# Kernel tuning notes

Measured on AMD Instinct MI355X. Metric: run time of the kernel, lower is better.

The kernel has to match this reference:

```python
import jax, jax.numpy as jnp
import numpy as np

N = 1_048_576
C = 64
K = 20
BN_EPS = 1e-3
IGNORE = -1


def setup_inputs() -> dict:
    key = jax.random.key(0)
    ks = jax.random.split(key, 8)
    feat = jax.random.normal(ks[0], (N, C), dtype=jnp.float32)
    coord = jax.random.uniform(ks[1], (N, 3), dtype=jnp.float32) * 10.0
    segment = jax.random.randint(ks[2], (N,), 0, K).astype(jnp.int32)
    instance = jax.random.randint(ks[3], (N,), 0, 500).astype(jnp.int32)
    instance_centroid = jax.random.uniform(ks[4], (N, 3), dtype=jnp.float32) * 10.0
    W1 = jax.random.normal(ks[5], (C, C), dtype=jnp.float32) * 0.05
    b1 = jnp.zeros((C,), jnp.float32)
    gamma = jnp.ones((C,), jnp.float32)
    beta = jnp.zeros((C,), jnp.float32)
    W2 = jax.random.normal(ks[6], (C, 3), dtype=jnp.float32) * 0.05
    b2 = jnp.zeros((3,), jnp.float32)
    Wseg = jax.random.normal(ks[7], (C, K), dtype=jnp.float32) * 0.05
    bseg = jnp.zeros((K,), jnp.float32)
    class_weights = jnp.ones((K,), jnp.float32)
    return dict(feat=feat, coord=coord, segment=segment, instance=instance,
                instance_centroid=instance_centroid, W1=W1, b1=b1, gamma=gamma,
                beta=beta, W2=W2, b2=b2, Wseg=Wseg, bseg=bseg,
                class_weights=class_weights)


def _heads(feat, W1, b1, gamma, beta, W2, b2, Wseg, bseg):
    # bias_head: Linear -> BatchNorm1d(train-mode batch stats, eps=1e-3) -> ReLU -> Linear
    h = feat @ W1 + b1                      # [N, C]
    mean = jnp.mean(h, axis=0)
    var = jnp.var(h, axis=0)                # biased var, matching torch BN
    h = (h - mean) * jax.lax.rsqrt(var + BN_EPS) * gamma + beta
    h = jax.nn.relu(h)
    bias_pred = h @ W2 + b2                 # [N, 3]
    logit_pred = feat @ Wseg + bseg         # [N, K]
    return logit_pred, bias_pred


def reference(feat, coord, segment, instance, instance_centroid,
              W1, b1, gamma, beta, W2, b2, Wseg, bseg, class_weights):
    logit_pred, bias_pred = _heads(feat, W1, b1, gamma, beta, W2, b2, Wseg, bseg)

    # weighted CrossEntropyLoss with ignore_index, torch semantics:
    # sum(w_t * nll) / sum(w_t) over non-ignored targets
    valid = (segment != IGNORE)
    tgt = jnp.where(valid, segment, 0)
    logp = jax.nn.log_softmax(logit_pred, axis=-1)
    nll = -jnp.take_along_axis(logp, tgt[:, None], axis=1)[:, 0]
    w = class_weights[tgt] * valid.astype(logp.dtype)
    seg_loss = jnp.sum(w * nll) / jnp.sum(w)

    mask = (instance != IGNORE).astype(bias_pred.dtype)
    denom = jnp.sum(mask) + 1e-8
    bias_gt = instance_centroid - coord
    bias_dist = jnp.sum(jnp.abs(bias_pred - bias_gt), axis=-1)
    bias_l1_loss = jnp.sum(bias_dist * mask) / denom

    pred_norm = bias_pred / (jnp.linalg.norm(bias_pred, axis=1, keepdims=True) + 1e-8)
    gt_norm = bias_gt / (jnp.linalg.norm(bias_gt, axis=1, keepdims=True) + 1e-8)
    cos = -jnp.sum(pred_norm * gt_norm, axis=-1)
    bias_cosine_loss = jnp.sum(cos * mask) / denom

    loss = seg_loss + bias_l1_loss + bias_cosine_loss
    return jnp.stack([loss, seg_loss, bias_l1_loss, bias_cosine_loss])
```

## Files before the change

### kernel.cpp

```cpp
#include <hip/hip_runtime.h>
#include <math.h>

#define C 64
#define K 20
#define TPB 256
#define ROWS_PER_TILE 128
#define NT 8
#define ASTR 72

#define NB 8
#define BSTR 512
#define SCOFF (NB * BSTR)
#define HOFF 18432

#define P1_TPB 128
#define P1_ROWS 128
#define LSTR 65

typedef __attribute__((ext_vector_type(8))) short bf16x8;
typedef __attribute__((ext_vector_type(4))) float f32x4;


__device__ __forceinline__ float wave_reduce_add(float v) {
#pragma unroll
  for (int m = 32; m > 0; m >>= 1) v += __shfl_xor(v, m, 64);
  return v;
}

__device__ __forceinline__ unsigned short f2bf16(float x) {
  union { float f; unsigned u; } v; v.f = x;
  unsigned r = v.u + 0x7FFFu + ((v.u >> 16) & 1u);
  return (unsigned short)(r >> 16);
}

__device__ __forceinline__ bf16x8 cvt8(float4 lo, float4 hi) {
  bf16x8 r;
  r[0] = (short)f2bf16(lo.x); r[1] = (short)f2bf16(lo.y);
  r[2] = (short)f2bf16(lo.z); r[3] = (short)f2bf16(lo.w);
  r[4] = (short)f2bf16(hi.x); r[5] = (short)f2bf16(hi.y);
  r[6] = (short)f2bf16(hi.z); r[7] = (short)f2bf16(hi.w);
  return r;
}



__global__ __launch_bounds__(TPB, 4)
void pass1_kernel(const float* __restrict__ feat,
                  const int* __restrict__ segment,
                  const float* __restrict__ W1,
                  const float* __restrict__ Wseg,
                  const float* __restrict__ bseg,
                  const float* __restrict__ cw,
                  float* __restrict__ ws,
                  unsigned short* __restrict__ hout,
                  int store_h, int n) {
  __shared__ __align__(16) unsigned short Bs[96 * ASTR];
  __shared__ float cred[512];
  __shared__ float wpart[8];

  const int t = threadIdx.x;
  const int wv = t >> 6;
  const int L = t & 63;
  const int colL = L & 15;
  const int quad = L >> 4;
  const long long blockbase = (long long)blockIdx.x * (ROWS_PER_TILE * NT);
  const int rbase = wv * 32;

  float* bucket = ws + (blockIdx.x & (NB - 1)) * BSTR;

  float s1[4] = {0, 0, 0, 0}, s2[4] = {0, 0, 0, 0};
  float wnll = 0.f, wsum = 0.f;

  const float bsega = bseg[colL];
  const float bsegb = (colL < 4) ? bseg[16 + colL] : 0.f;

  float4 af[8];
  auto issue_tile = [&](int it) {
    const long long trow = blockbase + (long long)it * ROWS_PER_TILE + rbase;
    const float* frow = feat + (trow + colL) * C + quad * 8;
#pragma unroll
    for (int rt = 0; rt < 2; ++rt)
#pragma unroll
      for (int kh = 0; kh < 2; ++kh) {
        const float* p = frow + rt * (16 * C) + kh * 32;
        af[rt * 4 + kh * 2 + 0] = *(const float4*)p;
        af[rt * 4 + kh * 2 + 1] = *(const float4*)(p + 4);
      }
  };

  issue_tile(0);

#pragma unroll
  for (int i = 0; i < 16; ++i) {
    int e = t + i * 256;
    Bs[(e & 63) * ASTR + (e >> 6)] = f2bf16(W1[e]);
  }
#pragma unroll
  for (int i = 0; i < 8; ++i) {
    int e = t + i * 256;
    int k = e >> 5, j = e & 31;
    float v = (j < K) ? Wseg[k * K + j] : 0.0f;
    Bs[(64 + j) * ASTR + k] = f2bf16(v);
  }
  __syncthreads();

  for (int it = 0; it < NT; ++it) {
    int segc[8];
    {
      const long long trow = blockbase + (long long)it * ROWS_PER_TILE + rbase;
#pragma unroll
      for (int rt = 0; rt < 2; ++rt)
#pragma unroll
        for (int r = 0; r < 4; ++r)
          segc[rt * 4 + r] = segment[trow + rt * 16 + quad * 4 + r];
    }

    bf16x8 a[2][2];
#pragma unroll
    for (int rt = 0; rt < 2; ++rt)
#pragma unroll
      for (int kh = 0; kh < 2; ++kh)
        a[rt][kh] = cvt8(af[rt * 4 + kh * 2], af[rt * 4 + kh * 2 + 1]);
    if (it + 1 < NT) issue_tile(it + 1);

    f32x4 ah[2][4];
#pragma unroll
    for (int rt = 0; rt < 2; ++rt)
#pragma unroll
      for (int ct = 0; ct < 4; ++ct) ah[rt][ct] = (f32x4){0.f, 0.f, 0.f, 0.f};
#pragma unroll
    for (int kh = 0; kh < 2; ++kh) {
      const int k0 = kh * 32 + quad * 8;
#pragma unroll
      for (int ct = 0; ct < 4; ++ct) {
        bf16x8 b = *(const bf16x8*)(Bs + (ct * 16 + colL) * ASTR + k0);
        ah[0][ct] = __builtin_amdgcn_mfma_f32_16x16x32_bf16(a[0][kh], b, ah[0][ct], 0, 0, 0);
        ah[1][ct] = __builtin_amdgcn_mfma_f32_16x16x32_bf16(a[1][kh], b, ah[1][ct], 0, 0, 0);
      }
    }

    {
      unsigned short* uso = hout + (long long)(blockIdx.x * NT + it) * 8192 + wv * 2048;
#pragma unroll
      for (int rt = 0; rt < 2; ++rt)
#pragma unroll
        for (int ct = 0; ct < 4; ++ct) {
          float v0 = ah[rt][ct][0], v1 = ah[rt][ct][1];
          float v2 = ah[rt][ct][2], v3 = ah[rt][ct][3];
          s1[ct] += v0 + v1 + v2 + v3;
          s2[ct] = __builtin_fmaf(v0, v0, s2[ct]);
          s2[ct] = __builtin_fmaf(v1, v1, s2[ct]);
          s2[ct] = __builtin_fmaf(v2, v2, s2[ct]);
          s2[ct] = __builtin_fmaf(v3, v3, s2[ct]);
          if (store_h) {
            ushort4 o;
            o.x = f2bf16(v0); o.y = f2bf16(v1); o.z = f2bf16(v2); o.w = f2bf16(v3);
            *(ushort4*)(uso + (rt * 4 + ct) * 256 + L * 4) = o;
          }
        }
    }

    f32x4 alg[2][2];
#pragma unroll
    for (int rt = 0; rt < 2; ++rt)
#pragma unroll
      for (int cc = 0; cc < 2; ++cc) alg[rt][cc] = (f32x4){0.f, 0.f, 0.f, 0.f};
#pragma unroll
    for (int kh = 0; kh < 2; ++kh) {
      const int k0 = kh * 32 + quad * 8;
#pragma unroll
      for (int cc = 0; cc < 2; ++cc) {
        bf16x8 b = *(const bf16x8*)(Bs + ((4 + cc) * 16 + colL) * ASTR + k0);
        alg[0][cc] = __builtin_amdgcn_mfma_f32_16x16x32_bf16(a[0][kh], b, alg[0][cc], 0, 0, 0);
        alg[1][cc] = __builtin_amdgcn_mfma_f32_16x16x32_bf16(a[1][kh], b, alg[1][cc], 0, 0, 0);
      }
    }

#pragma unroll
    for (int rt = 0; rt < 2; ++rt)
#pragma unroll
      for (int r = 0; r < 4; ++r) {
        float la = alg[rt][0][r] + bsega;
        float lb = (colL < 4) ? alg[rt][1][r] + bsegb : -3.0e38f;
        const int sg = segc[rt * 4 + r];
        const bool valid = (sg != -1);
        const int tgt = valid ? sg : 0;
        float mx = fmaxf(la, lb);
        mx = fmaxf(mx, __shfl_xor(mx, 1, 64));
        mx = fmaxf(mx, __shfl_xor(mx, 2, 64));
        mx = fmaxf(mx, __shfl_xor(mx, 4, 64));
        mx = fmaxf(mx, __shfl_xor(mx, 8, 64));
        float e = __expf(la - mx) + ((colL < 4) ? __expf(lb - mx) : 0.f);
        float tp = ((colL == tgt) ? la : 0.f) + ((colL + 16 == tgt) ? lb : 0.f);
#pragma unroll
        for (int m = 1; m <= 8; m <<= 1) {
          e += __shfl_xor(e, m, 64);
          tp += __shfl_xor(tp, m, 64);
        }
        float nll = mx + __logf(e) - tp;
        float wct = cw[tgt];
        if (colL == 0) {
          float w = valid ? wct : 0.f;
          wnll += w * nll;
          wsum += w;
        }
      }
  }

#pragma unroll
  for (int ct = 0; ct < 4; ++ct) {
    float a1 = s1[ct]; a1 += __shfl_xor(a1, 16, 64); a1 += __shfl_xor(a1, 32, 64);
    float a2 = s2[ct]; a2 += __shfl_xor(a2, 16, 64); a2 += __shfl_xor(a2, 32, 64);
    if (L < 16) { cred[wv * 64 + ct * 16 + colL] = a1; cred[256 + wv * 64 + ct * 16 + colL] = a2; }
  }
  {
    float rwn = wave_reduce_add(wnll);
    float rw = wave_reduce_add(wsum);
    if (L == 0) { wpart[wv * 2] = rwn; wpart[wv * 2 + 1] = rw; }
  }
  __syncthreads();
  if (t == 0) {
    atomicAdd(&bucket[0], wpart[0] + wpart[2] + wpart[4] + wpart[6]);
    atomicAdd(&bucket[1], wpart[1] + wpart[3] + wpart[5] + wpart[7]);
  }
  if (t < C) {
    float u1 = cred[t] + cred[64 + t] + cred[128 + t] + cred[192 + t];
    float u2 = cred[256 + t] + cred[320 + t] + cred[384 + t] + cred[448 + t];
    atomicAdd(&bucket[8 + t], u1);
    atomicAdd(&bucket[72 + t], u2);
  }
}


__global__ void prep_kernel(const float* __restrict__ gamma,
                            const float* __restrict__ beta,
                            float* __restrict__ ws, int n) {
  int j = threadIdx.x;
  float s1 = 0.f, s2 = 0.f;
#pragma unroll
  for (int b = 0; b < NB; ++b) { s1 += ws[b * BSTR + 8 + j]; s2 += ws[b * BSTR + 72 + j]; }
  float inv_n = 1.0f / (float)n;
  float mean = s1 * inv_n;
  float var = fmaxf(s2 * inv_n - mean * mean, 0.0f);
  float sc = gamma[j] * rsqrtf(var + 1e-3f);
  ws[SCOFF + j] = sc;
  ws[SCOFF + 64 + j] = beta[j] - mean * sc;
}


__global__ __launch_bounds__(TPB, 4)
void pass2_frag(const unsigned short* __restrict__ hsrc,
                const float* __restrict__ coord,
                const int* __restrict__ instance,
                const float* __restrict__ centroid,
                const float* __restrict__ W2,
                const float* __restrict__ b2,
                float* __restrict__ ws, int n) {
  __shared__ float part[4][3];
  const int t = threadIdx.x;
  const int w = t >> 6, L = t & 63;
  const int colL = L & 15, quad = L >> 4;
  float* bucket = ws + (blockIdx.x & (NB - 1)) * BSTR;

  const float* ssc = ws + SCOFF;
  const float* ssh = ws + SCOFF + 64;
  float scv[4], shv[4], w20[4], w21[4], w22[4];
#pragma unroll
  for (int ct = 0; ct < 4; ++ct) {
    int j = ct * 16 + colL;
    scv[ct] = ssc[j];
    shv[ct] = ssh[j];
    w20[ct] = W2[j * 3 + 0];
    w21[ct] = W2[j * 3 + 1];
    w22[ct] = W2[j * 3 + 2];
  }
  const float bb0 = b2[0], bb1 = b2[1], bb2 = b2[2];

  float l1a = 0.f, cosa = 0.f, ma = 0.f;

  ushort4 hv[8];
  auto issue_h = [&](int it) {
    const ushort4* src = (const ushort4*)(hsrc + (long long)(blockIdx.x * NT + it) * 8192 + w * 2048);
#pragma unroll
    for (int s = 0; s < 8; ++s) hv[s] = src[s * 64 + L];
  };
  float pc[2][3], pg[2][3]; int pin[2];
  auto issue_pts = [&](int it) {
    if (colL < 4) {
      const long long rowb = (long long)blockIdx.x * (ROWS_PER_TILE * NT) +
                             (long long)it * ROWS_PER_TILE + w * 32 + quad * 4 + colL;
#pragma unroll
      for (int rt = 0; rt < 2; ++rt) {
        long long p = rowb + rt * 16;
        pc[rt][0] = coord[p * 3 + 0]; pc[rt][1] = coord[p * 3 + 1]; pc[rt][2] = coord[p * 3 + 2];
        pg[rt][0] = centroid[p * 3 + 0]; pg[rt][1] = centroid[p * 3 + 1]; pg[rt][2] = centroid[p * 3 + 2];
        pin[rt] = instance[p];
      }
    }
  };

  issue_h(0);
  issue_pts(0);

  for (int it = 0; it < NT; ++it) {
    ushort4 hc[8];
#pragma unroll
    for (int s = 0; s < 8; ++s) hc[s] = hv[s];
    if (it + 1 < NT) issue_h(it + 1);

#pragma unroll
    for (int rt = 0; rt < 2; ++rt) {
      float d[12];
#pragma unroll
      for (int e = 0; e < 12; ++e) d[e] = 0.f;
#pragma unroll
      for (int ct = 0; ct < 4; ++ct) {
        ushort4 q = hc[rt * 4 + ct];
        unsigned short qa[4] = { q.x, q.y, q.z, q.w };
#pragma unroll
        for (int r = 0; r < 4; ++r) {
          float v = __uint_as_float((unsigned)qa[r] << 16);
          float y = fmaxf(__builtin_fmaf(v, scv[ct], shv[ct]), 0.0f);
          d[r * 3 + 0] = __builtin_fmaf(y, w20[ct], d[r * 3 + 0]);
          d[r * 3 + 1] = __builtin_fmaf(y, w21[ct], d[r * 3 + 1]);
          d[r * 3 + 2] = __builtin_fmaf(y, w22[ct], d[r * 3 + 2]);
        }
      }
#pragma unroll
      for (int m = 1; m <= 8; m <<= 1)
#pragma unroll
        for (int e = 0; e < 12; ++e) d[e] += __shfl_xor(d[e], m, 64);
      if (colL < 4) {
        const int r = colL;
        float bp0 = d[r * 3 + 0] + bb0;
        float bp1 = d[r * 3 + 1] + bb1;
        float bp2 = d[r * 3 + 2] + bb2;
        float gx = pg[rt][0] - pc[rt][0];
        float gy = pg[rt][1] - pc[rt][1];
        float gz = pg[rt][2] - pc[rt][2];
        float m = (pin[rt] != -1) ? 1.0f : 0.0f;
        float l1 = fabsf(bp0 - gx) + fabsf(bp1 - gy) + fabsf(bp2 - gz);
        float npn = sqrtf(bp0 * bp0 + bp1 * bp1 + bp2 * bp2) + 1e-8f;
        float ngn = sqrtf(gx * gx + gy * gy + gz * gz) + 1e-8f;
        float cs = -(bp0 * gx + bp1 * gy + bp2 * gz) / (npn * ngn);
        l1a += l1 * m;
        cosa += cs * m;
        ma += m;
      }
    }
    if (it + 1 < NT) issue_pts(it + 1);
  }

  float r0 = wave_reduce_add(l1a);
  float r1 = wave_reduce_add(cosa);
  float r2 = wave_reduce_add(ma);
  if (L == 0) { part[w][0] = r0; part[w][1] = r1; part[w][2] = r2; }
  __syncthreads();
  if (t == 0) {
    float a0 = 0, a1 = 0, a2 = 0;
#pragma unroll
    for (int k = 0; k < 4; ++k) { a0 += part[k][0]; a1 += part[k][1]; a2 += part[k][2]; }
    atomicAdd(&bucket[2], a0);
    atomicAdd(&bucket[3], a1);
    atomicAdd(&bucket[4], a2);
  }
}


__global__ __launch_bounds__(P1_TPB, 2)
void pass2_recompute(const float* __restrict__ feat,
                     const float* __restrict__ coord,
                     const int* __restrict__ instance,
                     const float* __restrict__ centroid,
                     const float* __restrict__ W1,
                     const float* __restrict__ W2,
                     const float* __restrict__ b2,
                     float* __restrict__ ws, int n) {
  __shared__ float lds[P1_ROWS * LSTR];
  __shared__ float part[2][3];
  const int tid = threadIdx.x;
  const int wave = tid >> 6;
  const int lane = tid & 63;
  const long long base = (long long)blockIdx.x * P1_ROWS;
  float* bucket = ws + (blockIdx.x & (NB - 1)) * BSTR;

  {
    const float4* src = (const float4*)(feat + base * C);
#pragma unroll
    for (int i = 0; i < 16; ++i) {
      int g = tid + i * P1_TPB;
      float4 v = src[g];
      float* d = &lds[(g >> 4) * LSTR + ((g & 15) << 2)];
      d[0] = v.x; d[1] = v.y; d[2] = v.z; d[3] = v.w;
    }
  }
  __syncthreads();

  float h[C];
#pragma unroll
  for (int j = 0; j < C; ++j) h[j] = 0.0f;
  const float* frow = &lds[tid * LSTR];
#pragma unroll 4
  for (int k = 0; k < C; ++k) {
    float fk = frow[k];
#pragma unroll
    for (int j = 0; j < C; ++j) h[j] = __builtin_fmaf(fk, W1[k * C + j], h[j]);
  }

  const float* ssc = ws + SCOFF;
  const float* ssh = ws + SCOFF + 64;
  float bp0 = b2[0], bp1 = b2[1], bp2 = b2[2];
#pragma unroll
  for (int j = 0; j < C; ++j) {
    float y = fmaxf(__builtin_fmaf(h[j], ssc[j], ssh[j]), 0.0f);
    bp0 = __builtin_fmaf(y, W2[j * 3 + 0], bp0);
    bp1 = __builtin_fmaf(y, W2[j * 3 + 1], bp1);
    bp2 = __builtin_fmaf(y, W2[j * 3 + 2], bp2);
  }

  const long long p = base + tid;
  float cx = coord[p * 3 + 0], cy = coord[p * 3 + 1], cz = coord[p * 3 + 2];
  float gx = centroid[p * 3 + 0] - cx;
  float gy = centroid[p * 3 + 1] - cy;
  float gz = centroid[p * 3 + 2] - cz;
  float m = (instance[p] != -1) ? 1.0f : 0.0f;
  float l1 = fabsf(bp0 - gx) + fabsf(bp1 - gy) + fabsf(bp2 - gz);
  float npn = sqrtf(bp0 * bp0 + bp1 * bp1 + bp2 * bp2) + 1e-8f;
  float ngn = sqrtf(gx * gx + gy * gy + gz * gz) + 1e-8f;
  float cs = -(bp0 * gx + bp1 * gy + bp2 * gz) / (npn * ngn);
  float r0 = wave_reduce_add(l1 * m);
  float r1 = wave_reduce_add(cs * m);
  float r2 = wave_reduce_add(m);
  if (lane == 0) { part[wave][0] = r0; part[wave][1] = r1; part[wave][2] = r2; }
  __syncthreads();
  if (tid == 0) {
    atomicAdd(&bucket[2], part[0][0] + part[1][0]);
    atomicAdd(&bucket[3], part[0][1] + part[1][1]);
    atomicAdd(&bucket[4], part[0][2] + part[1][2]);
  }
}


__global__ void finalize_kernel(const float* __restrict__ ws, float* __restrict__ out) {
  if (threadIdx.x == 0 && blockIdx.x == 0) {
    float a0 = 0, a1 = 0, a2 = 0, a3 = 0, a4 = 0;
#pragma unroll
    for (int b = 0; b < NB; ++b) {
      const float* bk = ws + b * BSTR;
      a0 += bk[0]; a1 += bk[1]; a2 += bk[2]; a3 += bk[3]; a4 += bk[4];
    }
    float seg = a0 / a1;
    float den = a4 + 1e-8f;
    float l1 = a2 / den;
    float cs = a3 / den;
    out[0] = seg + l1 + cs;
    out[1] = seg;
    out[2] = l1;
    out[3] = cs;
  }
}


extern "C" void kernel_launch(void* const* d_in, const int* in_sizes, int n_in,
                              void* d_out, int out_size, void* d_ws, size_t ws_size,
                              hipStream_t stream) {
  const float* feat = (const float*)d_in[0];
  const float* coord = (const float*)d_in[1];
  const int* segment = (const int*)d_in[2];
  const int* instance = (const int*)d_in[3];
  const float* centroid = (const float*)d_in[4];
  const float* W1 = (const float*)d_in[5];
  const float* gamma = (const float*)d_in[7];
  const float* beta = (const float*)d_in[8];
  const float* W2 = (const float*)d_in[9];
  const float* b2 = (const float*)d_in[10];
  const float* Wseg = (const float*)d_in[11];
  const float* bseg = (const float*)d_in[12];
  const float* cw = (const float*)d_in[13];

  const int n = in_sizes[0] / C;

  float* ws = (float*)d_ws;
  unsigned short* hbuf = (unsigned short*)((char*)d_ws + HOFF);
  const size_t need = (size_t)HOFF + (size_t)n * C * sizeof(unsigned short);
  const int store_h = (ws_size >= need) ? 1 : 0;

  size_t zbytes = ws_size < (size_t)(NB * BSTR * 4) ? ws_size : (size_t)(NB * BSTR * 4);
  hipMemsetAsync(d_ws, 0, zbytes, stream);

  const int nblk = n / (ROWS_PER_TILE * NT);
  pass1_kernel<<<nblk, TPB, 0, stream>>>(feat, segment, W1, Wseg, bseg, cw,
                                         ws, hbuf, store_h, n);
  prep_kernel<<<1, 64, 0, stream>>>(gamma, beta, ws, n);
  if (store_h) {
    pass2_frag<<<nblk, TPB, 0, stream>>>(hbuf, coord, instance, centroid,
                                         W2, b2, ws, n);
  } else {
    pass2_recompute<<<n / P1_ROWS, P1_TPB, 0, stream>>>(feat, coord, instance, centroid,
                                                        W1, W2, b2, ws, n);
  }
  finalize_kernel<<<1, 1, 0, stream>>>(ws, (float*)d_out);
}
```

Before: 564.1 us.

## Recompute BN-head hidden layer with MFMA in pass2 instead of storing bf16 h

Removes the bf16 h spill buffer that pass1 wrote and pass2 read back, and also removes the scalar-FMA recompute fallback. Pass2 now reloads feat, converts it to bf16 and recomputes feat@W1 with the same MFMA tiling pass1 uses before applying BN, ReLU and W2. This drops the write and read of an N×64 intermediate and the workspace-size dependence. In exchange it re-reads the full fp32 feat tensor and repeats the GEMM in pass2.

New measurement: 664.4 us. +17.8%, slower.

```diff
diff --git a/kernel.cpp b/kernel.cpp
--- a/kernel.cpp
+++ b/kernel.cpp
@@ -11,11 +11,6 @@
 #define NB 8
 #define BSTR 512
 #define SCOFF (NB * BSTR)
-#define HOFF 18432
-
-#define P1_TPB 128
-#define P1_ROWS 128
-#define LSTR 65
 
 typedef __attribute__((ext_vector_type(8))) short bf16x8;
 typedef __attribute__((ext_vector_type(4))) float f32x4;
@@ -51,9 +46,7 @@
                   const float* __restrict__ Wseg,
                   const float* __restrict__ bseg,
                   const float* __restrict__ cw,
-                  float* __restrict__ ws,
-                  unsigned short* __restrict__ hout,
-                  int store_h, int n) {
+                  float* __restrict__ ws, int n) {
   __shared__ __align__(16) unsigned short Bs[96 * ASTR];
   __shared__ float cred[512];
   __shared__ float wpart[8];
@@ -139,26 +132,18 @@
       }
     }
 
-    {
-      unsigned short* uso = hout + (long long)(blockIdx.x * NT + it) * 8192 + wv * 2048;
-#pragma unroll
-      for (int rt = 0; rt < 2; ++rt)
-#pragma unroll
-        for (int ct = 0; ct < 4; ++ct) {
-          float v0 = ah[rt][ct][0], v1 = ah[rt][ct][1];
-          float v2 = ah[rt][ct][2], v3 = ah[rt][ct][3];
-          s1[ct] += v0 + v1 + v2 + v3;
-          s2[ct] = __builtin_fmaf(v0, v0, s2[ct]);
-          s2[ct] = __builtin_fmaf(v1, v1, s2[ct]);
-          s2[ct] = __builtin_fmaf(v2, v2, s2[ct]);
-          s2[ct] = __builtin_fmaf(v3, v3, s2[ct]);
-          if (store_h) {
-            ushort4 o;
-            o.x = f2bf16(v0); o.y = f2bf16(v1); o.z = f2bf16(v2); o.w = f2bf16(v3);
-            *(ushort4*)(uso + (rt * 4 + ct) * 256 + L * 4) = o;
-          }
-        }
-    }
+#pragma unroll
+    for (int rt = 0; rt < 2; ++rt)
+#pragma unroll
+      for (int ct = 0; ct < 4; ++ct) {
+        float v0 = ah[rt][ct][0], v1 = ah[rt][ct][1];
+        float v2 = ah[rt][ct][2], v3 = ah[rt][ct][3];
+        s1[ct] += v0 + v1 + v2 + v3;
+        s2[ct] = __builtin_fmaf(v0, v0, s2[ct]);
+        s2[ct] = __builtin_fmaf(v1, v1, s2[ct]);
+        s2[ct] = __builtin_fmaf(v2, v2, s2[ct]);
+        s2[ct] = __builtin_fmaf(v3, v3, s2[ct]);
+      }
 
     f32x4 alg[2][2];
 #pragma unroll
@@ -249,17 +234,22 @@
 
 
 __global__ __launch_bounds__(TPB, 4)
-void pass2_frag(const unsigned short* __restrict__ hsrc,
+void pass2_mfma(const float* __restrict__ feat,
                 const float* __restrict__ coord,
                 const int* __restrict__ instance,
                 const float* __restrict__ centroid,
+                const float* __restrict__ W1,
                 const float* __restrict__ W2,
                 const float* __restrict__ b2,
                 float* __restrict__ ws, int n) {
+  __shared__ __align__(16) unsigned short Bs[64 * ASTR];
   __shared__ float part[4][3];
+
   const int t = threadIdx.x;
-  const int w = t >> 6, L = t & 63;
+  const int wv = t >> 6, L = t & 63;
   const int colL = L & 15, quad = L >> 4;
+  const long long blockbase = (long long)blockIdx.x * (ROWS_PER_TILE * NT);
+  const int rbase = wv * 32;
   float* bucket = ws + (blockIdx.x & (NB - 1)) * BSTR;
 
   const float* ssc = ws + SCOFF;
@@ -276,19 +266,24 @@
   }
   const float bb0 = b2[0], bb1 = b2[1], bb2 = b2[2];
 
-  float l1a = 0.f, cosa = 0.f, ma = 0.f;
-
-  ushort4 hv[8];
-  auto issue_h = [&](int it) {
-    const ushort4* src = (const ushort4*)(hsrc + (long long)(blockIdx.x * NT + it) * 8192 + w * 2048);
-#pragma unroll
-    for (int s = 0; s < 8; ++s) hv[s] = src[s * 64 + L];
+  float4 af[8];
+  auto issue_tile = [&](int it) {
+    const long long trow = blockbase + (long long)it * ROWS_PER_TILE + rbase;
+    const float* frow = feat + (trow + colL) * C + quad * 8;
+#pragma unroll
+    for (int rt = 0; rt < 2; ++rt)
+#pragma unroll
+      for (int kh = 0; kh < 2; ++kh) {
+        const float* p = frow + rt * (16 * C) + kh * 32;
+        af[rt * 4 + kh * 2 + 0] = *(const float4*)p;
+        af[rt * 4 + kh * 2 + 1] = *(const float4*)(p + 4);
+      }
   };
   float pc[2][3], pg[2][3]; int pin[2];
   auto issue_pts = [&](int it) {
     if (colL < 4) {
-      const long long rowb = (long long)blockIdx.x * (ROWS_PER_TILE * NT) +
-                             (long long)it * ROWS_PER_TILE + w * 32 + quad * 4 + colL;
+      const long long rowb = blockbase + (long long)it * ROWS_PER_TILE +
+                             rbase + quad * 4 + colL;
 #pragma unroll
       for (int rt = 0; rt < 2; ++rt) {
         long long p = rowb + rt * 16;
@@ -299,14 +294,43 @@
     }
   };
 
-  issue_h(0);
+  issue_tile(0);
+
+#pragma unroll
+  for (int i = 0; i < 16; ++i) {
+    int e = t + i * 256;
+    Bs[(e & 63) * ASTR + (e >> 6)] = f2bf16(W1[e]);
+  }
+  __syncthreads();
+
   issue_pts(0);
 
+  float l1a = 0.f, cosa = 0.f, ma = 0.f;
+
   for (int it = 0; it < NT; ++it) {
-    ushort4 hc[8];
-#pragma unroll
-    for (int s = 0; s < 8; ++s) hc[s] = hv[s];
-    if (it + 1 < NT) issue_h(it + 1);
+    bf16x8 a[2][2];
+#pragma unroll
+    for (int rt = 0; rt < 2; ++rt)
+#pragma unroll
+      for (int kh = 0; kh < 2; ++kh)
+        a[rt][kh] = cvt8(af[rt * 4 + kh * 2], af[rt * 4 + kh * 2 + 1]);
+    if (it + 1 < NT) issue_tile(it + 1);
+
+    f32x4 ah[2][4];
+#pragma unroll
+    for (int rt = 0; rt < 2; ++rt)
+#pragma unroll
+      for (int ct = 0; ct < 4; ++ct) ah[rt][ct] = (f32x4){0.f, 0.f, 0.f, 0.f};
+#pragma unroll
+    for (int kh = 0; kh < 2; ++kh) {
+      const int k0 = kh * 32 + quad * 8;
+#pragma unroll
+      for (int ct = 0; ct < 4; ++ct) {
+        bf16x8 b = *(const bf16x8*)(Bs + (ct * 16 + colL) * ASTR + k0);
+        ah[0][ct] = __builtin_amdgcn_mfma_f32_16x16x32_bf16(a[0][kh], b, ah[0][ct], 0, 0, 0);
+        ah[1][ct] = __builtin_amdgcn_mfma_f32_16x16x32_bf16(a[1][kh], b, ah[1][ct], 0, 0, 0);
+      }
+    }
 
 #pragma unroll
     for (int rt = 0; rt < 2; ++rt) {
@@ -315,11 +339,9 @@
       for (int e = 0; e < 12; ++e) d[e] = 0.f;
 #pragma unroll
       for (int ct = 0; ct < 4; ++ct) {
-        ushort4 q = hc[rt * 4 + ct];
-        unsigned short qa[4] = { q.x, q.y, q.z, q.w };
 #pragma unroll
         for (int r = 0; r < 4; ++r) {
-          float v = __uint_as_float((unsigned)qa[r] << 16);
+          float v = ah[rt][ct][r];
           float y = fmaxf(__builtin_fmaf(v, scv[ct], shv[ct]), 0.0f);
           d[r * 3 + 0] = __builtin_fmaf(y, w20[ct], d[r * 3 + 0]);
           d[r * 3 + 1] = __builtin_fmaf(y, w21[ct], d[r * 3 + 1]);
@@ -354,7 +376,7 @@
   float r0 = wave_reduce_add(l1a);
   float r1 = wave_reduce_add(cosa);
   float r2 = wave_reduce_add(ma);
-  if (L == 0) { part[w][0] = r0; part[w][1] = r1; part[w][2] = r2; }
+  if (L == 0) { part[wv][0] = r0; part[wv][1] = r1; part[wv][2] = r2; }
   __syncthreads();
   if (t == 0) {
     float a0 = 0, a1 = 0, a2 = 0;
@@ -363,80 +385,6 @@
     atomicAdd(&bucket[2], a0);
     atomicAdd(&bucket[3], a1);
     atomicAdd(&bucket[4], a2);
-  }
-}
-
-
-__global__ __launch_bounds__(P1_TPB, 2)
-void pass2_recompute(const float* __restrict__ feat,
-                     const float* __restrict__ coord,
-                     const int* __restrict__ instance,
-                     const float* __restrict__ centroid,
-                     const float* __restrict__ W1,
-                     const float* __restrict__ W2,
-                     const float* __restrict__ b2,
-                     float* __restrict__ ws, int n) {
-  __shared__ float lds[P1_ROWS * LSTR];
-  __shared__ float part[2][3];
-  const int tid = threadIdx.x;
-  const int wave = tid >> 6;
-  const int lane = tid & 63;
-  const long long base = (long long)blockIdx.x * P1_ROWS;
-  float* bucket = ws + (blockIdx.x & (NB - 1)) * BSTR;
-
-  {
-    const float4* src = (const float4*)(feat + base * C);
-#pragma unroll
-    for (int i = 0; i < 16; ++i) {
-      int g = tid + i * P1_TPB;
-      float4 v = src[g];
-      float* d = &lds[(g >> 4) * LSTR + ((g & 15) << 2)];
-      d[0] = v.x; d[1] = v.y; d[2] = v.z; d[3] = v.w;
-    }
-  }
-  __syncthreads();
-
-  float h[C];
-#pragma unroll
-  for (int j = 0; j < C; ++j) h[j] = 0.0f;
-  const float* frow = &lds[tid * LSTR];
-#pragma unroll 4
-  for (int k = 0; k < C; ++k) {
-    float fk = frow[k];
-#pragma unroll
-    for (int j = 0; j < C; ++j) h[j] = __builtin_fmaf(fk, W1[k * C + j], h[j]);
-  }
-
-  const float* ssc = ws + SCOFF;
-  const float* ssh = ws + SCOFF + 64;
-  float bp0 = b2[0], bp1 = b2[1], bp2 = b2[2];
-#pragma unroll
-  for (int j = 0; j < C; ++j) {
-    float y = fmaxf(__builtin_fmaf(h[j], ssc[j], ssh[j]), 0.0f);
-    bp0 = __builtin_fmaf(y, W2[j * 3 + 0], bp0);
-    bp1 = __builtin_fmaf(y, W2[j * 3 + 1], bp1);
-    bp2 = __builtin_fmaf(y, W2[j * 3 + 2], bp2);
-  }
-
-  const long long p = base + tid;
-  float cx = coord[p * 3 + 0], cy = coord[p * 3 + 1], cz = coord[p * 3 + 2];
-  float gx = centroid[p * 3 + 0] - cx;
-  float gy = centroid[p * 3 + 1] - cy;
-  float gz = centroid[p * 3 + 2] - cz;
-  float m = (instance[p] != -1) ? 1.0f : 0.0f;
-  float l1 = fabsf(bp0 - gx) + fabsf(bp1 - gy) + fabsf(bp2 - gz);
-  float npn = sqrtf(bp0 * bp0 + bp1 * bp1 + bp2 * bp2) + 1e-8f;
-  float ngn = sqrtf(gx * gx + gy * gy + gz * gz) + 1e-8f;
-  float cs = -(bp0 * gx + bp1 * gy + bp2 * gz) / (npn * ngn);
-  float r0 = wave_reduce_add(l1 * m);
-  float r1 = wave_reduce_add(cs * m);
-  float r2 = wave_reduce_add(m);
-  if (lane == 0) { part[wave][0] = r0; part[wave][1] = r1; part[wave][2] = r2; }
-  __syncthreads();
-  if (tid == 0) {
-    atomicAdd(&bucket[2], part[0][0] + part[1][0]);
-    atomicAdd(&bucket[3], part[0][1] + part[1][1]);
-    atomicAdd(&bucket[4], part[0][2] + part[1][2]);
   }
 }
 
@@ -481,23 +429,14 @@
   const int n = in_sizes[0] / C;
 
   float* ws = (float*)d_ws;
-  unsigned short* hbuf = (unsigned short*)((char*)d_ws + HOFF);
-  const size_t need = (size_t)HOFF + (size_t)n * C * sizeof(unsigned short);
-  const int store_h = (ws_size >= need) ? 1 : 0;
-
-  size_t zbytes = ws_size < (size_t)(NB * BSTR * 4) ? ws_size : (size_t)(NB * BSTR * 4);
+  size_t zmax = (size_t)(NB * BSTR * 4);
+  size_t zbytes = ws_size < zmax ? ws_size : zmax;
   hipMemsetAsync(d_ws, 0, zbytes, stream);
 
   const int nblk = n / (ROWS_PER_TILE * NT);
-  pass1_kernel<<<nblk, TPB, 0, stream>>>(feat, segment, W1, Wseg, bseg, cw,
-                                         ws, hbuf, store_h, n);
+  pass1_kernel<<<nblk, TPB, 0, stream>>>(feat, segment, W1, Wseg, bseg, cw, ws, n);
   prep_kernel<<<1, 64, 0, stream>>>(gamma, beta, ws, n);
-  if (store_h) {
-    pass2_frag<<<nblk, TPB, 0, stream>>>(hbuf, coord, instance, centroid,
-                                         W2, b2, ws, n);
-  } else {
-    pass2_recompute<<<n / P1_ROWS, P1_TPB, 0, stream>>>(feat, coord, instance, centroid,
-                                                        W1, W2, b2, ws, n);
-  }
+  pass2_mfma<<<nblk, TPB, 0, stream>>>(feat, coord, instance, centroid,
+                                       W1, W2, b2, ws, n);
   finalize_kernel<<<1, 1, 0, stream>>>(ws, (float*)d_out);
 }
```
